# Kernel tuning notes

Measured on AMD Instinct MI355X. Metric: run time of the kernel, lower is better.

Reference implementation:

```python
import jax, jax.numpy as jnp
import numpy as np

FEATURE_MAPS = [38, 19, 10, 5, 3, 1]
NUM_ANCHORS = [4, 6, 6, 6, 4, 4]
SCALES = (0.2, 0.9)
RATIOS = np.array([1.0, 1.0, 2.0, 3.0, 0.5, 1.0 / 3.0])
BACKGROUND_ID = 0
EPS = 1e-6


def _generate_anchors():
    """Replicates AnchorManager._generate_anchors: order is (i, j, k)."""
    all_anchors = []
    for size, n in zip(FEATURE_MAPS, NUM_ANCHORS):
        scales = np.linspace(SCALES[0], SCALES[1], n)
        ratios = RATIOS[:n]
        rs = np.sqrt(ratios)
        w = scales * rs          # [n]
        h = scales / rs          # [n]
        cy = (np.arange(size) + 0.5) / size  # i -> rows (varies slowest)
        cx = (np.arange(size) + 0.5) / size  # j -> cols
        grid = np.zeros((size, size, n, 4), dtype=np.float64)
        grid[..., 0] = cx[None, :, None]
        grid[..., 1] = cy[:, None, None]
        grid[..., 2] = w[None, None, :]
        grid[..., 3] = h[None, None, :]
        all_anchors.append(grid.reshape(-1, 4))
    return np.concatenate(all_anchors).astype(np.float32)  # [A, 4] cxcywh


def _cxcywh_to_xyxy(b):
    cxy, wh = b[..., :2], b[..., 2:]
    return jnp.concatenate([cxy - wh / 2, cxy + wh / 2], axis=-1)


def _xyxy_to_cxcywh(b):
    xy1, xy2 = b[..., :2], b[..., 2:]
    return jnp.concatenate([(xy1 + xy2) / 2, xy2 - xy1], axis=-1)


def setup_inputs() -> dict:
    key = jax.random.key(0)
    k1, k2, k3 = jax.random.split(key, 3)
    B, N = 64, 100
    # valid normalized xyxy gt boxes
    xy = jax.random.uniform(k1, (B, N, 2), dtype=jnp.float32) * 0.8
    wh = jax.random.uniform(k2, (B, N, 2), dtype=jnp.float32) * 0.19 + 0.01
    gt_boxes = jnp.concatenate([xy, xy + wh], axis=-1)
    gt_labels = jax.random.randint(k3, (B, N), 1, 81, dtype=jnp.int64 if jax.config.jax_enable_x64 else jnp.int32).astype(jnp.int32)
    anchors_cxcywh = jnp.asarray(_generate_anchors())          # [A, 4]
    anchors_xyxy = _cxcywh_to_xyxy(anchors_cxcywh)             # [A, 4]
    return {
        "gt_labels": gt_labels,
        "gt_boxes": gt_boxes,
        "anchors_cxcywh": anchors_cxcywh,
        "anchors_xyxy": anchors_xyxy,
    }


def _iou(anchors_xyxy, gt_boxes):
    # anchors_xyxy: [A,4], gt_boxes: [B,N,4] -> iou [B,A,N]
    a = anchors_xyxy[None, :, None, :]   # [1,A,1,4]
    g = gt_boxes[:, None, :, :]          # [B,1,N,4]
    lt = jnp.maximum(a[..., :2], g[..., :2])
    rb = jnp.minimum(a[..., 2:], g[..., 2:])
    wh = jnp.clip(rb - lt, 0.0)
    inter = wh[..., 0] * wh[..., 1]
    area_a = (a[..., 2] - a[..., 0]) * (a[..., 3] - a[..., 1])
    area_g = (g[..., 2] - g[..., 0]) * (g[..., 3] - g[..., 1])
    return (inter / (area_a + area_g - inter)).astype(jnp.float32)


def reference(gt_labels, gt_boxes, anchors_cxcywh, anchors_xyxy):
    B, N = gt_boxes.shape[0], gt_boxes.shape[1]
    A = anchors_cxcywh.shape[0]

    gt_boxes_coco = _xyxy_to_cxcywh(gt_boxes)                  # [B,N,4]
    ious = _iou(anchors_xyxy, gt_boxes)                        # [B,A,N]

    anchors_gt = jnp.max(ious, axis=-1)                        # [B,A]
    anchors_gt_idx = jnp.argmax(ious, axis=-1)                 # [B,A]
    gt_anchors_idx = jnp.argmax(ious, axis=-2)                 # [B,N] best anchor per gt

    # force-match: each gt claims its best anchor
    b_idx = jnp.arange(B)[:, None]
    range_n = jnp.broadcast_to(jnp.arange(N), (B, N))
    anchors_gt_idx = anchors_gt_idx.at[b_idx, gt_anchors_idx].set(range_n)
    anchors_gt = anchors_gt.at[b_idx, gt_anchors_idx].set(2.0)

    pos_mask = anchors_gt > 0.5                                # [B,A]

    matched_gtb = jnp.take_along_axis(gt_boxes_coco, anchors_gt_idx[..., None], axis=1)  # [B,A,4]
    matched_labels = jnp.take_along_axis(gt_labels, anchors_gt_idx, axis=1)              # [B,A]
    encoded_labels = jnp.where(pos_mask, matched_labels, BACKGROUND_ID)

    anc = anchors_cxcywh[None]                                 # [1,A,4]
    enc_cxy = (matched_gtb[..., :2] - anc[..., :2]) / anc[..., 2:]
    enc_wh = jnp.log((matched_gtb[..., 2:] + EPS) / (anc[..., 2:] + EPS))
    encoded = jnp.concatenate([enc_cxy, enc_wh], axis=-1)      # [B,A,4]

    return encoded_labels, encoded, pos_mask
```

## Files before the change

### kernel.cpp

```cpp
#include <hip/hip_runtime.h>
#include <math.h>

#pragma clang fp contract(off)


#define AA 8732
#define NN 100
#define BB 64
#define NTILE 35
#define EPS_F 1e-6f
#define OVR_FLAG 0x10000
#define POS_BIT  0x8000
#define DEFL 0.9999995f
#define RT_SEED 1e-38f

__constant__ int FM_SIZE[6] = {38, 19, 10, 5, 3, 1};
__constant__ int FM_NF[6]   = {4, 6, 6, 6, 4, 4};
__constant__ int FM_OFF[6]  = {0, 5776, 7942, 8542, 8692, 8728};

__device__ __forceinline__ void geom(const float4 axy, const float4 g,
                                     float area_a, float ag,
                                     float& inter, float& uni) {
    float ltx = fmaxf(axy.x, g.x);
    float lty = fmaxf(axy.y, g.y);
    float rbx = fminf(axy.z, g.z);
    float rby = fminf(axy.w, g.w);
    float w = fmaxf(rbx - ltx, 0.0f);
    float h = fmaxf(rby - lty, 0.0f);
    inter = w * h;
    uni = area_a + ag - inter;
}

__global__ void prior_kernel(const float4* __restrict__ gt_boxes,
                             const float4* __restrict__ anchors_xyxy,
                             unsigned long long* __restrict__ colmax,
                             float4* __restrict__ tab4) {
    const int b = blockIdx.x;
    const int n = threadIdx.x;
    if (n >= NN) return;
    float4 g = gt_boxes[b * NN + n];
    float ag = (g.z - g.x) * (g.w - g.y);
    float cx = (g.x + g.z) * 0.5f;
    float cy = (g.y + g.w) * 0.5f;
    float best = 0.0f;
    for (int f = 0; f < 6; f++) {
        int s = FM_SIZE[f];
        int j = (int)(cx * (float)s); j = j < s - 1 ? j : s - 1;
        int i = (int)(cy * (float)s); i = i < s - 1 ? i : s - 1;
        int base = FM_OFF[f] + (i * s + j) * FM_NF[f];
        for (int k = 0; k < FM_NF[f]; k++) {
            float4 an = anchors_xyxy[base + k];
            float area_a = (an.z - an.x) * (an.w - an.y);
            float inter, uni;
            geom(an, g, area_a, ag, inter, uni);
            best = fmaxf(best, inter * __builtin_amdgcn_rcpf(uni));
        }
    }
    float defl = best * DEFL;
    colmax[b * NN + n] = ((unsigned long long)__float_as_uint(defl)) << 32;
    tab4[(b * NN + n) * 2]     = g;
    tab4[(b * NN + n) * 2 + 1] = make_float4(ag, defl, 0.0f, 0.0f);
}

template <int N0, int N1>
__device__ __forceinline__ void passChunk(
        const float4 axy, const float area_a, const unsigned lowkey,
        const int tid,
        const float4* __restrict__ tb,
        float* tb_at,
        unsigned long long* __restrict__ cm,
        float& rt, unsigned& rm)
{
    #pragma unroll 4
    for (int n = N0; n < N1; n++) {
        float4 g = tb[n * 2];
        float4 q = tb[n * 2 + 1];
        float inter, uni;
        geom(axy, g, area_a, q.x, inter, uni);
        float qa = inter * __builtin_amdgcn_rcpf(uni);
        bool r = (qa >= rt);
        rt = fmaxf(rt, qa * DEFL);
        rm |= (r ? 1u : 0u) << (n - N0);
        if (__any((int)(qa >= q.y))) {
            float iou = inter / uni;
            bool cc = (qa >= q.y);
            unsigned long long p = cc
                ? ((((unsigned long long)__float_as_uint(iou)) << 32) |
                   (unsigned long long)lowkey) : 0ull;
            #pragma unroll
            for (int off = 32; off > 0; off >>= 1) {
                unsigned long long o = __shfl_xor(p, off);
                p = o > p ? o : p;
            }
            if ((tid & 63) == 0 && p != 0ull) {
                atomicMax(cm + n, p);
                atomicMax((unsigned*)(tb_at + n * 8 + 5),
                    __float_as_uint(
                        __uint_as_float((unsigned)(p >> 32)) * DEFL));
            }
        }
    }
}

__global__ __launch_bounds__(256, 8) void iou_smem_kernel(
        const float4* __restrict__ anchors_xyxy,
        const float4* __restrict__ tab_ro,
        float* tab_at,
        unsigned long long* __restrict__ colmax,
        int* __restrict__ out_slot)
{
    const int b = blockIdx.y;
    const int tid = threadIdx.x;
    const int a = blockIdx.x * 256 + tid;
    const bool valid = (a < AA);
    const int ac = valid ? a : (AA - 1);

    const float4* __restrict__ tb = tab_ro + (size_t)b * NN * 2;
    float* tbat = tab_at + (size_t)b * NN * 8;
    unsigned long long* cm = colmax + (size_t)b * NN;

    const float4 axy = anchors_xyxy[ac];
    const float area_a = (axy.z - axy.x) * (axy.w - axy.y);
    const unsigned lowkey = (unsigned)(AA - ac);

    float rt = RT_SEED;
    unsigned rm0 = 0, rm1 = 0, rm2 = 0, rm3 = 0;
    passChunk<0, 32>(axy, area_a, lowkey, tid, tb, tbat, cm, rt, rm0);
    passChunk<32, 64>(axy, area_a, lowkey, tid, tb, tbat, cm, rt, rm1);
    passChunk<64, 96>(axy, area_a, lowkey, tid, tb, tbat, cm, rt, rm2);
    passChunk<96, NN>(axy, area_a, lowkey, tid, tb, tbat, cm, rt, rm3);

    float bv = 0.0f;
    int bi = 0;
    unsigned rms[4] = {rm0, rm1, rm2, rm3};
    #pragma unroll
    for (int h = 0; h < 4; h++) {
        unsigned m = rms[h];
        const int nb = h * 32;
        while (m) {
            int n = __builtin_ctz(m) + nb;
            m &= m - 1;
            float inter, uni;
            geom(axy, tb[n * 2], area_a, tb[n * 2 + 1].x, inter, uni);
            float qa = inter * __builtin_amdgcn_rcpf(uni);
            if (qa >= rt) {
                float iou = inter / uni;
                if (iou > bv) { bv = iou; bi = n; }
            }
        }
    }

    if (valid) {
        out_slot[(size_t)b * AA + a] = bi | (bv > 0.5f ? POS_BIT : 0);
    }
}

__global__ __launch_bounds__(256) void encode_fused_kernel(
        const int* __restrict__ gt_labels,
        const float4* __restrict__ gt_boxes,
        const float4* __restrict__ anchors_cxcywh,
        const unsigned long long* __restrict__ colmax,
        float* __restrict__ out)
{
    const int b = blockIdx.y;
    const int tid = threadIdx.x;
    const int abase = blockIdx.x * 256;

    __shared__ float4 sg[NN];
    __shared__ int    slab[NN];
    __shared__ int    ovr[256];

    ovr[tid] = -1;
    if (tid < NN) {
        sg[tid]   = gt_boxes[b * NN + tid];
        slab[tid] = gt_labels[b * NN + tid];
    }
    __syncthreads();
    if (tid < NN) {
        unsigned long long v = colmax[b * NN + tid];
        unsigned low = (unsigned)(v & 0xFFFFFFFFull);
        if (low >= 1u && low <= (unsigned)AA) {
            int rel = (AA - (int)low) - abase;
            if (rel >= 0 && rel < 256) atomicMax(&ovr[rel], tid);
        }
    }
    __syncthreads();

    const int a = abase + tid;
    if (a >= AA) return;

    const size_t BA = (size_t)BB * AA;
    const size_t base = (size_t)b * AA + a;

    int s = ((const int*)(out + 5 * BA))[base];
    int o = ovr[tid];

    int idx; bool pos;
    if (o >= 0) { idx = o;          pos = true; }
    else        { idx = s & 0x7FFF; pos = (s & POS_BIT) != 0; }

    const float4 g = sg[idx];
    const float gcx = (g.x + g.z) * 0.5f;
    const float gcy = (g.y + g.w) * 0.5f;
    const float gw  = g.z - g.x;
    const float gh  = g.w - g.y;

    const float4 anc = anchors_cxcywh[a];
    const float ecx = (gcx - anc.x) / anc.z;
    const float ecy = (gcy - anc.y) / anc.w;
    const float ew  = logf((gw + EPS_F) / (anc.z + EPS_F));
    const float eh  = logf((gh + EPS_F) / (anc.w + EPS_F));

    out[base] = pos ? (float)slab[idx] : 0.0f;
    ((float4*)(out + BA))[base] = make_float4(ecx, ecy, ew, eh);
    out[5 * BA + base] = pos ? 1.0f : 0.0f;
}

__global__ void scatter_kernel(const unsigned long long* __restrict__ colmax,
                               int* __restrict__ out_slot) {
    const int b = blockIdx.x;
    const int n = threadIdx.x;
    if (n < NN) {
        unsigned long long v = colmax[b * NN + n];
        unsigned low = (unsigned)(v & 0xFFFFFFFFull);
        if (low >= 1u && low <= (unsigned)AA) {
            int idx = AA - (int)low;
            atomicMax(&out_slot[(size_t)b * AA + idx], OVR_FLAG + n);
        }
    }
}

__global__ __launch_bounds__(256) void encode_kernel(
        const int* __restrict__ gt_labels,
        const float4* __restrict__ gt_boxes,
        const float4* __restrict__ anchors_cxcywh,
        float* __restrict__ out)
{
    const int b = blockIdx.y;
    const int tid = threadIdx.x;
    const int a = blockIdx.x * 256 + tid;

    __shared__ float4 sg[NN];
    __shared__ int    slab[NN];
    if (tid < NN) {
        sg[tid]   = gt_boxes[b * NN + tid];
        slab[tid] = gt_labels[b * NN + tid];
    }
    __syncthreads();
    if (a >= AA) return;

    const size_t BA = (size_t)BB * AA;
    const size_t base = (size_t)b * AA + a;

    int s = ((const int*)(out + 5 * BA))[base];

    int idx; bool pos;
    if (s >= OVR_FLAG) { idx = s - OVR_FLAG;  pos = true; }
    else               { idx = s & 0x7FFF;    pos = (s & POS_BIT) != 0; }

    const float4 g = sg[idx];
    const float gcx = (g.x + g.z) * 0.5f;
    const float gcy = (g.y + g.w) * 0.5f;
    const float gw  = g.z - g.x;
    const float gh  = g.w - g.y;

    const float4 anc = anchors_cxcywh[a];
    const float ecx = (gcx - anc.x) / anc.z;
    const float ecy = (gcy - anc.y) / anc.w;
    const float ew  = logf((gw + EPS_F) / (anc.z + EPS_F));
    const float eh  = logf((gh + EPS_F) / (anc.w + EPS_F));

    out[base] = pos ? (float)slab[idx] : 0.0f;
    ((float4*)(out + BA))[base] = make_float4(ecx, ecy, ew, eh);
    out[5 * BA + base] = pos ? 1.0f : 0.0f;
}

extern "C" void kernel_launch(void* const* d_in, const int* in_sizes, int n_in,
                              void* d_out, int out_size, void* d_ws, size_t ws_size,
                              hipStream_t stream) {
    const int*    gt_labels    = (const int*)d_in[0];
    const float4* gt_boxes     = (const float4*)d_in[1];
    const float4* anchors_cxcy = (const float4*)d_in[2];
    const float4* anchors_xyxy = (const float4*)d_in[3];
    float* out = (float*)d_out;

    const size_t BA = (size_t)BB * AA;
    int* slot = (int*)(out + 5 * BA);

    const bool fused = (ws_size >= (size_t)(BB * NN * 8));
    unsigned long long* colmax = fused
        ? (unsigned long long*)d_ws
        : (unsigned long long*)(out + BA);
    float* tabf = out + BA + (size_t)BB * NN * 2;
    float4* tab4 = (float4*)tabf;

    prior_kernel<<<BB, 128, 0, stream>>>(gt_boxes, anchors_xyxy, colmax, tab4);

    dim3 grid(NTILE, BB);
    iou_smem_kernel<<<grid, 256, 0, stream>>>(anchors_xyxy, tab4, tabf,
                                              colmax, slot);
    if (fused) {
        encode_fused_kernel<<<grid, 256, 0, stream>>>(gt_labels, gt_boxes,
                                                      anchors_cxcy, colmax,
                                                      out);
    } else {
        scatter_kernel<<<BB, 128, 0, stream>>>(colmax, slot);
        encode_kernel<<<grid, 256, 0, stream>>>(gt_labels, gt_boxes,
                                                anchors_cxcy, out);
    }
}
```

Measured before the change: 131.4 us.

## Split GT columns across half-wavefronts with persistent tiles and per-lane atomics

Rewrites the IoU kernel so each anchor row is handled by two half-wavefront lanes, each covering 50 of the 100 GT boxes. A fixed 2048-block grid walks 32-row tiles spread evenly over all batch rows. The per-column wave-wide shuffle reductions inside the loop are replaced by candidate bitmasks, followed by per-lane atomicMax on the column maxima. The two halves merge their running threshold and best match with cross-half shuffles. This shortens the serial loop per thread and removes the branchy wave reductions, but can raise atomic traffic when many lanes are column candidates.

```diff
diff --git a/kernel.cpp b/kernel.cpp
--- a/kernel.cpp
+++ b/kernel.cpp
@@ -8,6 +8,7 @@
 #define NN 100
 #define BB 64
 #define NTILE 35
+#define NWT 17464
 #define EPS_F 1e-6f
 #define OVR_FLAG 0x10000
 #define POS_BIT  0x8000
@@ -62,17 +63,14 @@
     tab4[(b * NN + n) * 2 + 1] = make_float4(ag, defl, 0.0f, 0.0f);
 }
 
-template <int N0, int N1>
-__device__ __forceinline__ void passChunk(
-        const float4 axy, const float area_a, const unsigned lowkey,
-        const int tid,
-        const float4* __restrict__ tb,
-        float* tb_at,
-        unsigned long long* __restrict__ cm,
-        float& rt, unsigned& rm)
+__device__ __forceinline__ void chunk25(
+        const float4 axy, const float area_a,
+        const float4* __restrict__ tb, const int nbase,
+        float& rt, unsigned& rm, unsigned& cm)
 {
-    #pragma unroll 4
-    for (int n = N0; n < N1; n++) {
+    #pragma unroll 5
+    for (int i = 0; i < 25; i++) {
+        const int n = nbase + i;
         float4 g = tb[n * 2];
         float4 q = tb[n * 2 + 1];
         float inter, uni;
@@ -80,78 +78,95 @@
         float qa = inter * __builtin_amdgcn_rcpf(uni);
         bool r = (qa >= rt);
         rt = fmaxf(rt, qa * DEFL);
-        rm |= (r ? 1u : 0u) << (n - N0);
-        if (__any((int)(qa >= q.y))) {
-            float iou = inter / uni;
-            bool cc = (qa >= q.y);
-            unsigned long long p = cc
-                ? ((((unsigned long long)__float_as_uint(iou)) << 32) |
-                   (unsigned long long)lowkey) : 0ull;
-            #pragma unroll
-            for (int off = 32; off > 0; off >>= 1) {
-                unsigned long long o = __shfl_xor(p, off);
-                p = o > p ? o : p;
-            }
-            if ((tid & 63) == 0 && p != 0ull) {
-                atomicMax(cm + n, p);
-                atomicMax((unsigned*)(tb_at + n * 8 + 5),
-                    __float_as_uint(
-                        __uint_as_float((unsigned)(p >> 32)) * DEFL));
-            }
-        }
-    }
-}
-
-__global__ __launch_bounds__(256, 8) void iou_smem_kernel(
+        rm |= (r ? 1u : 0u) << i;
+        cm |= ((qa >= q.y) ? 1u : 0u) << i;
+    }
+}
+
+__global__ __launch_bounds__(256, 8) void iou_half_kernel(
         const float4* __restrict__ anchors_xyxy,
         const float4* __restrict__ tab_ro,
         float* tab_at,
         unsigned long long* __restrict__ colmax,
         int* __restrict__ out_slot)
 {
-    const int b = blockIdx.y;
-    const int tid = threadIdx.x;
-    const int a = blockIdx.x * 256 + tid;
-    const bool valid = (a < AA);
-    const int ac = valid ? a : (AA - 1);
-
-    const float4* __restrict__ tb = tab_ro + (size_t)b * NN * 2;
-    float* tbat = tab_at + (size_t)b * NN * 8;
-    unsigned long long* cm = colmax + (size_t)b * NN;
-
-    const float4 axy = anchors_xyxy[ac];
-    const float area_a = (axy.z - axy.x) * (axy.w - axy.y);
-    const unsigned lowkey = (unsigned)(AA - ac);
-
-    float rt = RT_SEED;
-    unsigned rm0 = 0, rm1 = 0, rm2 = 0, rm3 = 0;
-    passChunk<0, 32>(axy, area_a, lowkey, tid, tb, tbat, cm, rt, rm0);
-    passChunk<32, 64>(axy, area_a, lowkey, tid, tb, tbat, cm, rt, rm1);
-    passChunk<64, 96>(axy, area_a, lowkey, tid, tb, tbat, cm, rt, rm2);
-    passChunk<96, NN>(axy, area_a, lowkey, tid, tb, tbat, cm, rt, rm3);
-
-    float bv = 0.0f;
-    int bi = 0;
-    unsigned rms[4] = {rm0, rm1, rm2, rm3};
-    #pragma unroll
-    for (int h = 0; h < 4; h++) {
-        unsigned m = rms[h];
-        const int nb = h * 32;
-        while (m) {
-            int n = __builtin_ctz(m) + nb;
-            m &= m - 1;
-            float inter, uni;
-            geom(axy, tb[n * 2], area_a, tb[n * 2 + 1].x, inter, uni);
-            float qa = inter * __builtin_amdgcn_rcpf(uni);
-            if (qa >= rt) {
+    const int tid  = threadIdx.x;
+    const int lane = tid & 63;
+    const int slot = blockIdx.x * 4 + (tid >> 6);
+    const int t0 = (slot * NWT) >> 13;
+    const int t1 = ((slot + 1) * NWT) >> 13;
+    const int lrow = lane & 31;
+    const int h    = lane >> 5;
+    const int n0   = h * 50;
+
+    for (int t = t0; t < t1; t++) {
+        const int r = t * 32 + lrow;
+        const int b = r / AA;
+        const int a = r - b * AA;
+        const float4 axy = anchors_xyxy[a];
+        const float area_a = (axy.z - axy.x) * (axy.w - axy.y);
+        const unsigned lowkey = (unsigned)(AA - a);
+        const float4* __restrict__ tb = tab_ro + (size_t)b * NN * 2;
+        float* tbat = tab_at + (size_t)b * NN * 8;
+        unsigned long long* cmx = colmax + (size_t)b * NN;
+
+        float rt = RT_SEED;
+        unsigned rm0 = 0, cm0 = 0, rm1 = 0, cm1 = 0;
+        chunk25(axy, area_a, tb, n0,      rt, rm0, cm0);
+        chunk25(axy, area_a, tb, n0 + 25, rt, rm1, cm1);
+
+        unsigned cms[2] = {cm0, cm1};
+        #pragma unroll
+        for (int hh = 0; hh < 2; hh++) {
+            unsigned c = cms[hh];
+            const int nb = n0 + hh * 25;
+            while (c) {
+                int n = __builtin_ctz(c) + nb;
+                c &= c - 1;
+                float inter, uni;
+                geom(axy, tb[n * 2], area_a, tb[n * 2 + 1].x, inter, uni);
                 float iou = inter / uni;
-                if (iou > bv) { bv = iou; bi = n; }
+                atomicMax(cmx + n,
+                    (((unsigned long long)__float_as_uint(iou)) << 32) |
+                    (unsigned long long)lowkey);
+                atomicMax((unsigned*)(tbat + n * 8 + 5),
+                          __float_as_uint(iou * DEFL));
             }
         }
-    }
-
-    if (valid) {
-        out_slot[(size_t)b * AA + a] = bi | (bv > 0.5f ? POS_BIT : 0);
+
+        rt = fmaxf(rt, __shfl_xor(rt, 32));
+
+        float bv = 0.0f;
+        int bi = 0;
+        unsigned rms[2] = {rm0, rm1};
+        #pragma unroll
+        for (int hh = 0; hh < 2; hh++) {
+            unsigned m = rms[hh];
+            const int nb = n0 + hh * 25;
+            while (m) {
+                int n = __builtin_ctz(m) + nb;
+                m &= m - 1;
+                float inter, uni;
+                geom(axy, tb[n * 2], area_a, tb[n * 2 + 1].x, inter, uni);
+                float qa = inter * __builtin_amdgcn_rcpf(uni);
+                if (qa >= rt) {
+                    float iou = inter / uni;
+                    if (iou > bv) { bv = iou; bi = n; }
+                }
+            }
+        }
+
+        unsigned long long k =
+            (((unsigned long long)__float_as_uint(bv)) << 32) |
+            (unsigned long long)(unsigned)(NN - bi);
+        unsigned long long o = __shfl_xor(k, 32);
+        k = o > k ? o : k;
+
+        if (h == 0) {
+            float fbv = __uint_as_float((unsigned)(k >> 32));
+            int   fbi = NN - (int)(k & 0xFFFFFFFFull);
+            out_slot[(size_t)b * AA + a] = fbi | (fbv > 0.5f ? POS_BIT : 0);
+        }
     }
 }
 
@@ -296,16 +311,17 @@
 
     prior_kernel<<<BB, 128, 0, stream>>>(gt_boxes, anchors_xyxy, colmax, tab4);
 
-    dim3 grid(NTILE, BB);
-    iou_smem_kernel<<<grid, 256, 0, stream>>>(anchors_xyxy, tab4, tabf,
+    iou_half_kernel<<<2048, 256, 0, stream>>>(anchors_xyxy, tab4, tabf,
                                               colmax, slot);
+
+    dim3 egrid(NTILE, BB);
     if (fused) {
-        encode_fused_kernel<<<grid, 256, 0, stream>>>(gt_labels, gt_boxes,
-                                                      anchors_cxcy, colmax,
-                                                      out);
+        encode_fused_kernel<<<egrid, 256, 0, stream>>>(gt_labels, gt_boxes,
+                                                       anchors_cxcy, colmax,
+                                                       out);
     } else {
         scatter_kernel<<<BB, 128, 0, stream>>>(colmax, slot);
-        encode_kernel<<<grid, 256, 0, stream>>>(gt_labels, gt_boxes,
-                                                anchors_cxcy, out);
-    }
-}
+        encode_kernel<<<egrid, 256, 0, stream>>>(gt_labels, gt_boxes,
+                                                 anchors_cxcy, out);
+    }
+}
```

Result: slower. 170.8 us (+29.9%).

## Split IoU work into balanced anchor-tile by GT-chunk units across waves

Applied to the files above, without the earlier changes.

Replaces the per-anchor-thread IoU kernel with a flat 2048-block grid in which each wavefront handles balanced units of 64 anchors by 25 ground-truth boxes. Per-chunk best matches are merged through shared-memory 64-bit atomicMax keyed on IoU and lowest index. This is intended to remove tail imbalance and improve occupancy. In exchange it loses the running-threshold pruning across chunks and adds LDS atomics and index arithmetic. The loop unroll factor is also changed to 5.

```diff
diff --git a/kernel.cpp b/kernel.cpp
--- a/kernel.cpp
+++ b/kernel.cpp
@@ -7,6 +7,9 @@
 #define AA 8732
 #define NN 100
 #define BB 64
+#define TPB 137
+#define NTILES (BB * TPB)
+#define NBLK 2048
 #define NTILE 35
 #define EPS_F 1e-6f
 #define OVR_FLAG 0x10000
@@ -65,13 +68,13 @@
 template <int N0, int N1>
 __device__ __forceinline__ void passChunk(
         const float4 axy, const float area_a, const unsigned lowkey,
-        const int tid,
+        const int lane,
         const float4* __restrict__ tb,
         float* tb_at,
         unsigned long long* __restrict__ cm,
         float& rt, unsigned& rm)
 {
-    #pragma unroll 4
+    #pragma unroll 5
     for (int n = N0; n < N1; n++) {
         float4 g = tb[n * 2];
         float4 q = tb[n * 2 + 1];
@@ -92,7 +95,7 @@
                 unsigned long long o = __shfl_xor(p, off);
                 p = o > p ? o : p;
             }
-            if ((tid & 63) == 0 && p != 0ull) {
+            if (lane == 0 && p != 0ull) {
                 atomicMax(cm + n, p);
                 atomicMax((unsigned*)(tb_at + n * 8 + 5),
                     __float_as_uint(
@@ -102,56 +105,98 @@
     }
 }
 
-__global__ __launch_bounds__(256, 8) void iou_smem_kernel(
+__global__ __launch_bounds__(256, 8) void iou_tile_kernel(
         const float4* __restrict__ anchors_xyxy,
         const float4* __restrict__ tab_ro,
         float* tab_at,
         unsigned long long* __restrict__ colmax,
         int* __restrict__ out_slot)
 {
-    const int b = blockIdx.y;
-    const int tid = threadIdx.x;
-    const int a = blockIdx.x * 256 + tid;
-    const bool valid = (a < AA);
-    const int ac = valid ? a : (AA - 1);
-
-    const float4* __restrict__ tb = tab_ro + (size_t)b * NN * 2;
-    float* tbat = tab_at + (size_t)b * NN * 8;
-    unsigned long long* cm = colmax + (size_t)b * NN;
-
-    const float4 axy = anchors_xyxy[ac];
-    const float area_a = (axy.z - axy.x) * (axy.w - axy.y);
-    const unsigned lowkey = (unsigned)(AA - ac);
-
-    float rt = RT_SEED;
-    unsigned rm0 = 0, rm1 = 0, rm2 = 0, rm3 = 0;
-    passChunk<0, 32>(axy, area_a, lowkey, tid, tb, tbat, cm, rt, rm0);
-    passChunk<32, 64>(axy, area_a, lowkey, tid, tb, tbat, cm, rt, rm1);
-    passChunk<64, 96>(axy, area_a, lowkey, tid, tb, tbat, cm, rt, rm2);
-    passChunk<96, NN>(axy, area_a, lowkey, tid, tb, tbat, cm, rt, rm3);
-
-    float bv = 0.0f;
-    int bi = 0;
-    unsigned rms[4] = {rm0, rm1, rm2, rm3};
-    #pragma unroll
-    for (int h = 0; h < 4; h++) {
-        unsigned m = rms[h];
-        const int nb = h * 32;
-        while (m) {
-            int n = __builtin_ctz(m) + nb;
-            m &= m - 1;
-            float inter, uni;
-            geom(axy, tb[n * 2], area_a, tb[n * 2 + 1].x, inter, uni);
-            float qa = inter * __builtin_amdgcn_rcpf(uni);
-            if (qa >= rt) {
-                float iou = inter / uni;
-                if (iou > bv) { bv = iou; bi = n; }
+    const int b0   = blockIdx.x;
+    const int tid  = threadIdx.x;
+    const int lane = tid & 63;
+    const int w    = tid >> 6;
+    const int t_lo = (b0 * TPB) >> 5;
+    const int t_hi = ((b0 + 1) * TPB) >> 5;
+    const int ntl  = t_hi - t_lo;
+    const int nm   = ntl * 4;
+    const int u_lo = (w * nm) >> 2;
+    const int u_hi = ((w + 1) * nm) >> 2;
+
+    __shared__ unsigned long long lmax[5 * 64];
+    for (int i = tid; i < ntl * 64; i += 256) lmax[i] = 0ull;
+    __syncthreads();
+
+    int m = u_lo;
+    while (m < u_hi) {
+        const int ts   = m >> 2;
+        const int c_lo = m & 3;
+        const int mend = min(u_hi, (ts + 1) * 4);
+        const int c_hi = c_lo + (mend - m);
+        const int tt   = t_lo + ts;
+        const int b    = tt / TPB;
+        const int trel = tt - b * TPB;
+        const int a    = trel * 64 + lane;
+        const int ac   = a < AA ? a : (AA - 1);
+        const float4 axy = anchors_xyxy[ac];
+        const float area_a = (axy.z - axy.x) * (axy.w - axy.y);
+        const unsigned lowkey = (unsigned)(AA - ac);
+        const float4* __restrict__ tb = tab_ro + (size_t)b * NN * 2;
+        float* tbat = tab_at + (size_t)b * NN * 8;
+        unsigned long long* cmx = colmax + (size_t)b * NN;
+
+        float rt = RT_SEED;
+        unsigned rm0 = 0, rm1 = 0, rm2 = 0, rm3 = 0;
+        if (c_lo == 0)             passChunk< 0, 25>(axy, area_a, lowkey,
+                                       lane, tb, tbat, cmx, rt, rm0);
+        if (c_lo <= 1 && c_hi > 1) passChunk<25, 50>(axy, area_a, lowkey,
+                                       lane, tb, tbat, cmx, rt, rm1);
+        if (c_lo <= 2 && c_hi > 2) passChunk<50, 75>(axy, area_a, lowkey,
+                                       lane, tb, tbat, cmx, rt, rm2);
+        if (c_hi > 3)              passChunk<75,100>(axy, area_a, lowkey,
+                                       lane, tb, tbat, cmx, rt, rm3);
+
+        float bv = 0.0f;
+        int bi = 0;
+        unsigned rms[4] = {rm0, rm1, rm2, rm3};
+        #pragma unroll
+        for (int h = 0; h < 4; h++) {
+            unsigned mm = rms[h];
+            const int nb = h * 25;
+            while (mm) {
+                int n = __builtin_ctz(mm) + nb;
+                mm &= mm - 1;
+                float inter, uni;
+                geom(axy, tb[n * 2], area_a, tb[n * 2 + 1].x, inter, uni);
+                float qa = inter * __builtin_amdgcn_rcpf(uni);
+                if (qa >= rt) {
+                    float iou = inter / uni;
+                    if (iou > bv) { bv = iou; bi = n; }
+                }
             }
         }
-    }
-
-    if (valid) {
-        out_slot[(size_t)b * AA + a] = bi | (bv > 0.5f ? POS_BIT : 0);
+
+        unsigned long long k =
+            (((unsigned long long)__float_as_uint(bv)) << 32) |
+            (unsigned long long)(unsigned)(NN - bi);
+        atomicMax(&lmax[ts * 64 + lane], k);
+
+        m = mend;
+    }
+    __syncthreads();
+
+    for (int i = tid; i < ntl * 64; i += 256) {
+        const int ts = i >> 6, ln = i & 63;
+        const int tt = t_lo + ts;
+        const int b  = tt / TPB;
+        const int trel = tt - b * TPB;
+        const int a  = trel * 64 + ln;
+        if (a < AA) {
+            unsigned long long k = lmax[i];
+            float fbv = __uint_as_float((unsigned)(k >> 32));
+            int   fbi = NN - (int)(k & 0xFFFFFFFFull);
+            out_slot[(size_t)b * AA + a] = fbi | (fbv > 0.5f ? POS_BIT : 0);
+        }
     }
 }
 
@@ -296,16 +341,17 @@
 
     prior_kernel<<<BB, 128, 0, stream>>>(gt_boxes, anchors_xyxy, colmax, tab4);
 
-    dim3 grid(NTILE, BB);
-    iou_smem_kernel<<<grid, 256, 0, stream>>>(anchors_xyxy, tab4, tabf,
+    iou_tile_kernel<<<NBLK, 256, 0, stream>>>(anchors_xyxy, tab4, tabf,
                                               colmax, slot);
+
+    dim3 egrid(NTILE, BB);
     if (fused) {
-        encode_fused_kernel<<<grid, 256, 0, stream>>>(gt_labels, gt_boxes,
-                                                      anchors_cxcy, colmax,
-                                                      out);
+        encode_fused_kernel<<<egrid, 256, 0, stream>>>(gt_labels, gt_boxes,
+                                                       anchors_cxcy, colmax,
+                                                       out);
     } else {
         scatter_kernel<<<BB, 128, 0, stream>>>(colmax, slot);
-        encode_kernel<<<grid, 256, 0, stream>>>(gt_labels, gt_boxes,
-                                                anchors_cxcy, out);
-    }
-}
+        encode_kernel<<<egrid, 256, 0, stream>>>(gt_labels, gt_boxes,
+                                                 anchors_cxcy, out);
+    }
+}
```

Result: slower. 201.4 us (+53.2%).
